# Kernel optimization log

Hardware: AMD Instinct MI355X
Metric: run time of the kernel (lower is better)

The kernel has to match this reference:

```python
import jax, jax.numpy as jnp
import numpy as np

NUM_HEADS = 32
HEAD_DIM = 512
EPS = 1e-12  # torch F.normalize eps


def setup_inputs() -> dict:
    key = jax.random.key(0)
    k1, k2, k3, k4, k5 = jax.random.split(key, 5)
    B, C, H, W = 32, 256, 64, 64
    return {
        "X": jax.random.normal(k1, (B, C, H, W), dtype=jnp.float32),
        "qkv_w": jax.random.normal(k2, (3 * HEAD_DIM, C), dtype=jnp.float32) * 0.02,
        "qkv_b": jax.random.normal(k3, (3 * HEAD_DIM,), dtype=jnp.float32) * 0.02,
        "proj_w": jax.random.normal(k4, (C, HEAD_DIM), dtype=jnp.float32) * 0.02,
        "proj_b": jax.random.normal(k5, (C,), dtype=jnp.float32) * 0.02,
    }


def _l2norm_axis1(x):
    # torch F.normalize(x, dim=1): x / max(||x||_2, eps)
    n = jnp.sqrt(jnp.sum(x * x, axis=1, keepdims=True))
    return x / jnp.maximum(n, EPS)


def reference(X, qkv_w, qkv_b, proj_w, proj_b):
    B, C, H, W = X.shape
    # 1x1 conv == channel matmul: [B,3*hd,H,W]
    qkv = jnp.einsum('bchw,oc->bohw', X, qkv_w) + qkv_b[None, :, None, None]
    # reshape to (B, 3, num_heads, head_dim, L) where L = H*W // num_heads
    qkv = qkv.reshape(B, 3, NUM_HEADS, HEAD_DIM, -1)
    q, k, v = qkv[:, 0], qkv[:, 1], qkv[:, 2]  # [B, nh, hd, L]
    # normalize across the num_heads axis (dim=1), as in the original code
    q = _l2norm_axis1(q)
    k = _l2norm_axis1(k)
    # attn = q^T @ k : [B, nh, L, L]
    attn = jnp.einsum('bhdl,bhdm->bhlm', q, k)
    attn = jax.nn.softmax(attn, axis=-1)
    # output = v @ attn^T : [B, nh, hd, L]
    out = jnp.einsum('bhdm,bhlm->bhdl', v, attn)
    out = out.reshape(B, HEAD_DIM, H, W)
    # proj 1x1 conv back to C channels
    out = jnp.einsum('bdhw,cd->bchw', out, proj_w) + proj_b[None, :, None, None]
    return out
```

## Files before the change

### kernel.cpp

```cpp
#include <hip/hip_runtime.h>
#include <stdint.h>


typedef float     f32x4   __attribute__((ext_vector_type(4)));
typedef short     bf16x8  __attribute__((ext_vector_type(8)));
typedef float     floatx4 __attribute__((ext_vector_type(4)));
typedef uint16_t  ushortx8 __attribute__((ext_vector_type(8)));
typedef uint16_t  ushortx4 __attribute__((ext_vector_type(4)));

#define DEVI static __device__ __forceinline__

DEVI float bf2f(uint16_t u) { union { uint32_t i; float f; } x; x.i = ((uint32_t)u) << 16; return x.f; }
DEVI uint16_t f2bf(float f) {
  union { float f; uint32_t i; } x; x.f = f;
  uint32_t r = x.i + 0x7fff + ((x.i >> 16) & 1);
  return (uint16_t)(r >> 16);
}

DEVI void gload16(const void* g, void* l) {
  __builtin_amdgcn_global_load_lds((const __attribute__((address_space(1))) void*)g,
                                   (__attribute__((address_space(3))) void*)l, 16, 0, 0);
}

DEVI float redmax16(float v) {
  v = fmaxf(v, __shfl_xor(v, 1)); v = fmaxf(v, __shfl_xor(v, 2));
  v = fmaxf(v, __shfl_xor(v, 4)); v = fmaxf(v, __shfl_xor(v, 8));
  return v;
}
DEVI float redsum16(float v) {
  v += __shfl_xor(v, 1); v += __shfl_xor(v, 2);
  v += __shfl_xor(v, 4); v += __shfl_xor(v, 8);
  return v;
}

__global__ __launch_bounds__(256) void k_transpose_x(const float* __restrict__ X,
                                                     uint16_t* __restrict__ Xt) {
  __shared__ float tile[64][65];
  int t = threadIdx.x;
  int st = blockIdx.x, ct = blockIdx.y, b = blockIdx.z;
  int row = t >> 2, cq = t & 3;
  const float* src = X + ((size_t)(b * 256 + ct * 64 + row)) * 4096 + st * 64 + cq * 16;
#pragma unroll
  for (int k = 0; k < 4; ++k) {
    floatx4 v = *(const floatx4*)(src + k * 4);
    tile[row][cq * 16 + k * 4 + 0] = v[0];
    tile[row][cq * 16 + k * 4 + 1] = v[1];
    tile[row][cq * 16 + k * 4 + 2] = v[2];
    tile[row][cq * 16 + k * 4 + 3] = v[3];
  }
  __syncthreads();
  int srow = t >> 2, oq = t & 3;
  ushortx8 o0, o1;
#pragma unroll
  for (int k = 0; k < 8; ++k) o0[k] = f2bf(tile[oq * 16 + k][srow]);
#pragma unroll
  for (int k = 0; k < 8; ++k) o1[k] = f2bf(tile[oq * 16 + 8 + k][srow]);
  uint16_t* dst = Xt + ((size_t)(b * 4096 + st * 64 + srow)) * 256 + ct * 64 + oq * 16;
  *(ushortx8*)dst = o0;
  *(ushortx8*)(dst + 8) = o1;
}

__global__ __launch_bounds__(256) void k_cvt_bf16(const float* __restrict__ src,
                                                  uint16_t* __restrict__ dst, int n) {
  int i = (blockIdx.x * 256 + threadIdx.x) * 4;
  if (i >= n) return;
  floatx4 v = *(const floatx4*)(src + i);
  ushortx4 o;
  o[0] = f2bf(v[0]); o[1] = f2bf(v[1]); o[2] = f2bf(v[2]); o[3] = f2bf(v[3]);
  *(ushortx4*)(dst + i) = o;
}

__global__ __launch_bounds__(256) void k_qkv_gemm(const uint16_t* __restrict__ W,
                                                  const uint16_t* __restrict__ Xt,
                                                  const float* __restrict__ bias_g,
                                                  uint16_t* __restrict__ qkv) {
  __shared__ __align__(16) uint16_t As[128 * 64];
  __shared__ __align__(16) uint16_t Bs[128 * 64];
  int t = threadIdx.x, lane = t & 63, wave = t >> 6;
  int st = blockIdx.x, ot = blockIdx.y, b = blockIdx.z;
  int wr = wave >> 1, wc = wave & 1;
  f32x4 acc[4][4] = {};
  int srow = lane >> 3;
  int sc_us = ((((lane & 7) * 16) ^ ((srow & 7) << 4)) >> 1);
  const uint16_t* Ag = W + (size_t)(ot * 128 + wave * 8 + srow) * 256;
  const uint16_t* Bg = Xt + ((size_t)(b * 4096 + st * 128 + wave * 8 + srow)) * 256;

  for (int kc = 0; kc < 4; ++kc) {
    __syncthreads();
#pragma unroll
    for (int c = 0; c < 4; ++c) {
      gload16(Ag + (size_t)(c * 32) * 256 + kc * 64 + sc_us, &As[(c * 32 + wave * 8) * 64]);
      gload16(Bg + (size_t)(c * 32) * 256 + kc * 64 + sc_us, &Bs[(c * 32 + wave * 8) * 64]);
    }
    __syncthreads();
#pragma unroll
    for (int kk = 0; kk < 2; ++kk) {
      bf16x8 a[4], bw[4];
#pragma unroll
      for (int i = 0; i < 4; ++i) {
        int r = wr * 64 + i * 16 + (lane & 15);
        a[i] = *(const bf16x8*)&As[r * 64 + ((kk * 32 + (lane >> 4) * 8) ^ ((r & 7) << 3))];
      }
#pragma unroll
      for (int j = 0; j < 4; ++j) {
        int r = wc * 64 + j * 16 + (lane & 15);
        bw[j] = *(const bf16x8*)&Bs[r * 64 + ((kk * 32 + (lane >> 4) * 8) ^ ((r & 7) << 3))];
      }
#pragma unroll
      for (int i = 0; i < 4; ++i)
#pragma unroll
        for (int j = 0; j < 4; ++j)
          acc[i][j] = __builtin_amdgcn_mfma_f32_16x16x32_bf16(a[i], bw[j], acc[i][j], 0, 0, 0);
    }
  }
  int o0 = ot * 128 + wr * 64, s0 = st * 128 + wc * 64;
  float bv[4][4];
#pragma unroll
  for (int i = 0; i < 4; ++i)
#pragma unroll
    for (int r = 0; r < 4; ++r) bv[i][r] = bias_g[o0 + i * 16 + (lane >> 4) * 4 + r];
#pragma unroll
  for (int i = 0; i < 4; ++i)
#pragma unroll
    for (int j = 0; j < 4; ++j)
#pragma unroll
      for (int r = 0; r < 4; ++r) {
        int o = o0 + i * 16 + (lane >> 4) * 4 + r;
        int s = s0 + j * 16 + (lane & 15);
        qkv[((size_t)b * 1536 + o) * 4096 + s] = f2bf(acc[i][j][r] + bv[i][r]);
      }
}

__global__ __launch_bounds__(256) void k_scales(const uint16_t* __restrict__ qkv,
                                                float* __restrict__ scaleB) {
  int t = threadIdx.x;
  int sc = blockIdx.x, g = blockIdx.y, b = blockIdx.z;
  const uint16_t* base = qkv + ((size_t)(b * 1536 + g * 512)) * 4096;
  float* sb = scaleB + ((size_t)(b * 2 + g)) * 16 * 4096;
  int c16 = t >> 4, so = t & 15;
  int s = sc * 128 + so * 8;
  float ss[8] = {};
  for (int h = 0; h < 32; ++h) {
    ushortx8 v = *(const ushortx8*)(base + ((size_t)(h * 16 + c16)) * 4096 + s);
#pragma unroll
    for (int j = 0; j < 8; ++j) { float f = bf2f(v[j]); ss[j] += f * f; }
  }
  floatx4 o0, o1;
#pragma unroll
  for (int j = 0; j < 4; ++j) o0[j] = 1.0f / fmaxf(sqrtf(ss[j]), 1e-12f);
#pragma unroll
  for (int j = 0; j < 4; ++j) o1[j] = 1.0f / fmaxf(sqrtf(ss[4 + j]), 1e-12f);
  *(floatx4*)(sb + c16 * 4096 + s) = o0;
  *(floatx4*)(sb + c16 * 4096 + s + 4) = o1;
}

__global__ __launch_bounds__(256) void k_apply(const uint16_t* __restrict__ qkv,
                                               const float* __restrict__ scaleB,
                                               uint16_t* __restrict__ Qp,
                                               uint16_t* __restrict__ Kp) {
  int t = threadIdx.x;
  int shc = blockIdx.x, h = blockIdx.y, z = blockIdx.z;
  int b = z >> 1, g = z & 1;
  const uint16_t* base = qkv + ((size_t)(b * 1536 + g * 512 + h * 16)) * 4096;
  const float* sb = scaleB + ((size_t)(b * 2 + g)) * 16 * 4096;
  uint16_t* dst = (g ? Kp : Qp) + (size_t)b * 32 * 65536 + (size_t)h * 65536;
#pragma unroll
  for (int k = 0; k < 4; ++k) {
    int id = k * 256 + t;
    int l = id & 127, od = id >> 7;
    ushortx8 o;
#pragma unroll
    for (int jj = 0; jj < 8; ++jj) {
      int dp = od * 8 + jj;
      int c16 = dp & 15;
      int s = (shc * 4 + (dp >> 4)) * 128 + l;
      float v = bf2f(base[(size_t)c16 * 4096 + s]);
      o[jj] = f2bf(v * sb[c16 * 4096 + s]);
    }
    *(ushortx8*)(dst + (size_t)l * 512 + shc * 64 + od * 8) = o;
  }
}

__global__ __launch_bounds__(256) void k_attn(const uint16_t* __restrict__ Qp,
                                              const uint16_t* __restrict__ Kp,
                                              const uint16_t* qkv,
                                              uint16_t* OtBase) {
  __shared__ __align__(16) uint16_t smemA[16384];
  __shared__ __align__(16) uint16_t Pb[16384];
  __shared__ float rsum[128];
  int t = threadIdx.x, lane = t & 63, w = t >> 6;
  int h = blockIdx.x, b = blockIdx.y;
  const size_t bh = (size_t)(b * 32 + h);
  const uint16_t* Qg = Qp + bh * 65536;
  const uint16_t* Kg = Kp + bh * 65536;
  uint16_t* QT = smemA;
  uint16_t* KT = smemA + 8192;
  int srow = lane >> 3;
  int sc_us = ((((lane & 7) * 16) ^ ((srow & 7) << 4)) >> 1);

  f32x4 accs[2][8] = {};
  for (int kc = 0; kc < 8; ++kc) {
    __syncthreads();
#pragma unroll
    for (int c = 0; c < 4; ++c) {
      int r = c * 32 + w * 8 + srow;
      gload16(Qg + (size_t)r * 512 + kc * 64 + sc_us, &QT[(c * 32 + w * 8) * 64]);
      gload16(Kg + (size_t)r * 512 + kc * 64 + sc_us, &KT[(c * 32 + w * 8) * 64]);
    }
    __syncthreads();
#pragma unroll
    for (int kk = 0; kk < 2; ++kk) {
      bf16x8 aq[2];
#pragma unroll
      for (int lf = 0; lf < 2; ++lf) {
        int r = w * 32 + lf * 16 + (lane & 15);
        aq[lf] = *(const bf16x8*)&QT[r * 64 + ((kk * 32 + (lane >> 4) * 8) ^ ((r & 7) << 3))];
      }
#pragma unroll
      for (int mf = 0; mf < 8; ++mf) {
        int r = mf * 16 + (lane & 15);
        bf16x8 bk = *(const bf16x8*)&KT[r * 64 + ((kk * 32 + (lane >> 4) * 8) ^ ((r & 7) << 3))];
        accs[0][mf] = __builtin_amdgcn_mfma_f32_16x16x32_bf16(aq[0], bk, accs[0][mf], 0, 0, 0);
        accs[1][mf] = __builtin_amdgcn_mfma_f32_16x16x32_bf16(aq[1], bk, accs[1][mf], 0, 0, 0);
      }
    }
  }

#pragma unroll
  for (int lf = 0; lf < 2; ++lf) {
#pragma unroll
    for (int r = 0; r < 4; ++r) {
      float mx = accs[lf][0][r];
#pragma unroll
      for (int mf = 1; mf < 8; ++mf) mx = fmaxf(mx, accs[lf][mf][r]);
      mx = redmax16(mx);
      float sum = 0.f;
#pragma unroll
      for (int mf = 0; mf < 8; ++mf) {
        float e = __expf(accs[lf][mf][r] - mx);
        accs[lf][mf][r] = e;
        sum += e;
      }
      sum = redsum16(sum);
      int l = w * 32 + lf * 16 + (lane >> 4) * 4 + r;
      if ((lane & 15) == 0) rsum[l] = 1.0f / sum;
#pragma unroll
      for (int mf = 0; mf < 8; ++mf) {
        int m = mf * 16 + (lane & 15);
        Pb[l * 128 + (m ^ ((l & 7) << 3))] = f2bf(accs[lf][mf][r]);
      }
    }
  }
  __syncthreads();

  uint16_t* Vt = smemA;
  const uint16_t* vg = qkv + ((size_t)(b * 1536 + 1024 + h * 16)) * 4096;
  int vrow = lane >> 2;
  int vcol_us = ((((lane & 3) * 16) ^ ((vrow & 3) << 4)) >> 1);
  uint16_t* OtB = OtBase + (size_t)b * 6291456;

#pragma unroll
  for (int lc = 0; lc < 2; ++lc) {
    f32x4 acco[8][4] = {};
    for (int mc = 0; mc < 4; ++mc) {
      __syncthreads();
#pragma unroll
      for (int c = 0; c < 8; ++c) {
        int d = c * 64 + w * 16 + vrow;
        gload16(vg + (size_t)(d >> 5) * 4096 + (d & 31) * 128 + mc * 32 + vcol_us,
                &Vt[(c * 64 + w * 16) * 32]);
      }
      __syncthreads();
      bf16x8 av[8], bp[4];
#pragma unroll
      for (int df = 0; df < 8; ++df) {
        int r = w * 128 + df * 16 + (lane & 15);
        av[df] = *(const bf16x8*)&Vt[r * 32 + (((lane >> 4) * 8) ^ ((r & 3) << 3))];
      }
#pragma unroll
      for (int lf = 0; lf < 4; ++lf) {
        int l = lc * 64 + lf * 16 + (lane & 15);
        bp[lf] = *(const bf16x8*)&Pb[l * 128 + ((mc * 32 + (lane >> 4) * 8) ^ ((l & 7) << 3))];
      }
#pragma unroll
      for (int df = 0; df < 8; ++df)
#pragma unroll
        for (int lf = 0; lf < 4; ++lf)
          acco[df][lf] = __builtin_amdgcn_mfma_f32_16x16x32_bf16(av[df], bp[lf], acco[df][lf], 0, 0, 0);
    }
    float scl[4];
#pragma unroll
    for (int lf = 0; lf < 4; ++lf) scl[lf] = rsum[lc * 64 + lf * 16 + (lane & 15)];

#pragma unroll
    for (int half = 0; half < 2; ++half) {
      __syncthreads();
#pragma unroll
      for (int df = 0; df < 8; ++df)
#pragma unroll
        for (int lf2 = 0; lf2 < 2; ++lf2) {
          int lf = half * 2 + lf2;
          int lloc = lf2 * 16 + (lane & 15);
#pragma unroll
          for (int r = 0; r < 4; ++r) {
            int d = w * 128 + df * 16 + (lane >> 4) * 4 + r;
            Vt[(lloc * 32 + (d & 31)) * 16 + (d >> 5)] = f2bf(acco[df][lf][r] * scl[lf]);
          }
        }
      __syncthreads();
#pragma unroll
      for (int i = 0; i < 4; ++i) {
        int chunk = i * 256 + t;
        int lloc = chunk >> 5, dlo = chunk & 31;
        int l = lc * 64 + half * 32 + lloc;
        ushortx8 v0 = *(ushortx8*)&Vt[chunk * 16];
        ushortx8 v1 = *(ushortx8*)&Vt[chunk * 16 + 8];
        uint16_t* gp = OtB + ((size_t)(dlo * 128 + l)) * 512 + h * 16;
        *(ushortx8*)gp = v0;
        *(ushortx8*)(gp + 8) = v1;
      }
    }
  }
}

__global__ __launch_bounds__(256) void k_proj_gemm(const uint16_t* __restrict__ Wp,
                                                   const uint16_t* __restrict__ Ot,
                                                   const float* __restrict__ bias_g,
                                                   float* __restrict__ outp) {
  __shared__ __align__(16) uint16_t As[128 * 64];
  __shared__ __align__(16) uint16_t Bs[128 * 64];
  int t = threadIdx.x, lane = t & 63, wave = t >> 6;
  int st = blockIdx.x, ct = blockIdx.y, b = blockIdx.z;
  int wr = wave >> 1, wc = wave & 1;
  f32x4 acc[4][4] = {};
  int srow = lane >> 3;
  int sc_us = ((((lane & 7) * 16) ^ ((srow & 7) << 4)) >> 1);
  const uint16_t* Ag = Wp + (size_t)(ct * 128 + wave * 8 + srow) * 512;
  const uint16_t* Bg = Ot + (size_t)b * 6291456 + ((size_t)(st * 128 + wave * 8 + srow)) * 512;

  for (int kc = 0; kc < 8; ++kc) {
    __syncthreads();
#pragma unroll
    for (int c = 0; c < 4; ++c) {
      gload16(Ag + (size_t)(c * 32) * 512 + kc * 64 + sc_us, &As[(c * 32 + wave * 8) * 64]);
      gload16(Bg + (size_t)(c * 32) * 512 + kc * 64 + sc_us, &Bs[(c * 32 + wave * 8) * 64]);
    }
    __syncthreads();
#pragma unroll
    for (int kk = 0; kk < 2; ++kk) {
      bf16x8 a[4], bw[4];
#pragma unroll
      for (int i = 0; i < 4; ++i) {
        int r = wr * 64 + i * 16 + (lane & 15);
        a[i] = *(const bf16x8*)&As[r * 64 + ((kk * 32 + (lane >> 4) * 8) ^ ((r & 7) << 3))];
      }
#pragma unroll
      for (int j = 0; j < 4; ++j) {
        int r = wc * 64 + j * 16 + (lane & 15);
        bw[j] = *(const bf16x8*)&Bs[r * 64 + ((kk * 32 + (lane >> 4) * 8) ^ ((r & 7) << 3))];
      }
#pragma unroll
      for (int i = 0; i < 4; ++i)
#pragma unroll
        for (int j = 0; j < 4; ++j)
          acc[i][j] = __builtin_amdgcn_mfma_f32_16x16x32_bf16(a[i], bw[j], acc[i][j], 0, 0, 0);
    }
  }
  int c0 = ct * 128 + wr * 64, s0 = st * 128 + wc * 64;
  float bv[4][4];
#pragma unroll
  for (int i = 0; i < 4; ++i)
#pragma unroll
    for (int r = 0; r < 4; ++r) bv[i][r] = bias_g[c0 + i * 16 + (lane >> 4) * 4 + r];
#pragma unroll
  for (int i = 0; i < 4; ++i)
#pragma unroll
    for (int j = 0; j < 4; ++j)
#pragma unroll
      for (int r = 0; r < 4; ++r) {
        int c = c0 + i * 16 + (lane >> 4) * 4 + r;
        int s = s0 + j * 16 + (lane & 15);
        outp[((size_t)b * 256 + c) * 4096 + s] = acc[i][j][r] + bv[i][r];
      }
}

extern "C" void kernel_launch(void* const* d_in, const int* in_sizes, int n_in,
                              void* d_out, int out_size, void* d_ws, size_t ws_size,
                              hipStream_t stream) {
  const float* X      = (const float*)d_in[0];
  const float* qkv_w  = (const float*)d_in[1];
  const float* qkv_b  = (const float*)d_in[2];
  const float* proj_w = (const float*)d_in[3];
  const float* proj_b = (const float*)d_in[4];
  float* outp = (float*)d_out;

  const size_t SZ_XT  = 2097152;
  const size_t SZ_QKV = 12582912;
  const size_t SZ_QP  = 4194304;
  const size_t SZ_W   = 786432 + 262144;

  int NB = 0;
  const int cand[6] = {32, 16, 8, 4, 2, 1};
  for (int ci = 0; ci < 6; ++ci) {
    size_t need = SZ_W + (size_t)cand[ci] * (SZ_XT + SZ_QKV + 2 * SZ_QP);
    if (need <= ws_size) { NB = cand[ci]; break; }
  }
  if (NB == 0) return;

  char* ws = (char*)d_ws;
  uint16_t* Wqb  = (uint16_t*)(ws);
  uint16_t* Wpb  = (uint16_t*)(ws + 786432);
  char*     gbuf = ws + SZ_W;
  uint16_t* Xt   = (uint16_t*)(gbuf);
  uint16_t* qkvb = (uint16_t*)(gbuf + (size_t)NB * SZ_XT);
  uint16_t* Qp   = (uint16_t*)(gbuf + (size_t)NB * (SZ_XT + SZ_QKV));
  uint16_t* Kp   = (uint16_t*)(gbuf + (size_t)NB * (SZ_XT + SZ_QKV + SZ_QP));
  float*    scaleB = (float*)Xt;

  k_cvt_bf16<<<dim3(384), 256, 0, stream>>>(qkv_w, Wqb, 1536 * 256);
  k_cvt_bf16<<<dim3(128), 256, 0, stream>>>(proj_w, Wpb, 256 * 512);

  for (int b0 = 0; b0 < 32; b0 += NB) {
    const float* Xg   = X + (size_t)b0 * 256 * 4096;
    float*       outg = outp + (size_t)b0 * 256 * 4096;
    k_transpose_x<<<dim3(64, 4, NB), 256, 0, stream>>>(Xg, Xt);
    k_qkv_gemm<<<dim3(32, 12, NB), 256, 0, stream>>>(Wqb, Xt, qkv_b, qkvb);
    k_scales<<<dim3(32, 2, NB), 256, 0, stream>>>(qkvb, scaleB);
    k_apply<<<dim3(8, 32, 2 * NB), 256, 0, stream>>>(qkvb, scaleB, Qp, Kp);
    k_attn<<<dim3(32, NB), 256, 0, stream>>>(Qp, Kp, qkvb, qkvb );
    k_proj_gemm<<<dim3(32, 2, NB), 256, 0, stream>>>(Wpb, qkvb , proj_b, outg);
  }
}
```

Before: 671.0 us.

## Fuse Q/K normalization into attention and write output in channel-major layout

Removes the separate k_apply pass and its Qp/Kp buffers. The attention kernel now reads bf16 Q/K straight from the qkv buffer, scales them by the precomputed inverse norms and writes them swizzled into LDS. The attention block grows to 512 threads, each wave owning 16 query rows and 64 head dims. The output is written directly in the original channel-major layout without an LDS transpose, and the projection GEMM gathers it with strided scalar loads. This saves a global round trip of Q/K but replaces vectorized async loads with 2-byte scalar gathers in both attention and projection.

Result: faster. 585.2 us (-12.8%).

```diff
diff --git a/kernel.cpp b/kernel.cpp
--- a/kernel.cpp
+++ b/kernel.cpp
@@ -136,7 +136,7 @@
   int t = threadIdx.x;
   int sc = blockIdx.x, g = blockIdx.y, b = blockIdx.z;
   const uint16_t* base = qkv + ((size_t)(b * 1536 + g * 512)) * 4096;
-  float* sb = scaleB + ((size_t)(b * 2 + g)) * 16 * 4096;
+  float* sb = scaleB + (size_t)b * 524288 + (size_t)g * 65536;
   int c16 = t >> 4, so = t & 15;
   int s = sc * 128 + so * 8;
   float ss[8] = {};
@@ -154,177 +154,137 @@
   *(floatx4*)(sb + c16 * 4096 + s + 4) = o1;
 }
 
-__global__ __launch_bounds__(256) void k_apply(const uint16_t* __restrict__ qkv,
-                                               const float* __restrict__ scaleB,
-                                               uint16_t* __restrict__ Qp,
-                                               uint16_t* __restrict__ Kp) {
-  int t = threadIdx.x;
-  int shc = blockIdx.x, h = blockIdx.y, z = blockIdx.z;
-  int b = z >> 1, g = z & 1;
-  const uint16_t* base = qkv + ((size_t)(b * 1536 + g * 512 + h * 16)) * 4096;
-  const float* sb = scaleB + ((size_t)(b * 2 + g)) * 16 * 4096;
-  uint16_t* dst = (g ? Kp : Qp) + (size_t)b * 32 * 65536 + (size_t)h * 65536;
-#pragma unroll
-  for (int k = 0; k < 4; ++k) {
-    int id = k * 256 + t;
-    int l = id & 127, od = id >> 7;
-    ushortx8 o;
-#pragma unroll
-    for (int jj = 0; jj < 8; ++jj) {
-      int dp = od * 8 + jj;
-      int c16 = dp & 15;
-      int s = (shc * 4 + (dp >> 4)) * 128 + l;
-      float v = bf2f(base[(size_t)c16 * 4096 + s]);
-      o[jj] = f2bf(v * sb[c16 * 4096 + s]);
-    }
-    *(ushortx8*)(dst + (size_t)l * 512 + shc * 64 + od * 8) = o;
-  }
-}
-
-__global__ __launch_bounds__(256) void k_attn(const uint16_t* __restrict__ Qp,
-                                              const uint16_t* __restrict__ Kp,
-                                              const uint16_t* qkv,
-                                              uint16_t* OtBase) {
+__global__ __launch_bounds__(512, 4) void k_attn(const uint16_t* __restrict__ qkv,
+                                                 const float* __restrict__ scaleB,
+                                                 uint16_t* OtAll) {
   __shared__ __align__(16) uint16_t smemA[16384];
   __shared__ __align__(16) uint16_t Pb[16384];
   __shared__ float rsum[128];
   int t = threadIdx.x, lane = t & 63, w = t >> 6;
   int h = blockIdx.x, b = blockIdx.y;
-  const size_t bh = (size_t)(b * 32 + h);
-  const uint16_t* Qg = Qp + bh * 65536;
-  const uint16_t* Kg = Kp + bh * 65536;
+  const uint16_t* qg = qkv + ((size_t)(b * 1536) + h * 16) * 4096;
+  const uint16_t* kg = qkv + ((size_t)(b * 1536) + 512 + h * 16) * 4096;
+  const float* sq = scaleB + (size_t)b * 524288;
+  const float* sk = sq + 65536;
   uint16_t* QT = smemA;
   uint16_t* KT = smemA + 8192;
-  int srow = lane >> 3;
-  int sc_us = ((((lane & 7) * 16) ^ ((srow & 7) << 4)) >> 1);
-
-  f32x4 accs[2][8] = {};
+
+  int sl = t & 127;
+  int dd8a = t >> 7;
+
+  f32x4 accs[8] = {};
   for (int kc = 0; kc < 8; ++kc) {
     __syncthreads();
 #pragma unroll
-    for (int c = 0; c < 4; ++c) {
-      int r = c * 32 + w * 8 + srow;
-      gload16(Qg + (size_t)r * 512 + kc * 64 + sc_us, &QT[(c * 32 + w * 8) * 64]);
-      gload16(Kg + (size_t)r * 512 + kc * 64 + sc_us, &KT[(c * 32 + w * 8) * 64]);
+    for (int kq = 0; kq < 2; ++kq) {
+      int dd8 = dd8a + kq * 4;
+      int c16 = kc * 2 + (dd8 >> 2);
+      int s0 = (dd8 & 3) * 8;
+      const uint16_t* qrow = qg + (size_t)c16 * 4096 + sl;
+      const uint16_t* krow = kg + (size_t)c16 * 4096 + sl;
+      const float* sqr = sq + c16 * 4096 + sl;
+      const float* skr = sk + c16 * 4096 + sl;
+      ushortx8 oq, ok;
+#pragma unroll
+      for (int j = 0; j < 8; ++j) {
+        int soff = (s0 + j) * 128;
+        oq[j] = f2bf(bf2f(qrow[soff]) * sqr[soff]);
+        ok[j] = f2bf(bf2f(krow[soff]) * skr[soff]);
+      }
+      int lidx = sl * 64 + ((dd8 * 8) ^ ((sl & 7) << 3));
+      *(ushortx8*)&QT[lidx] = oq;
+      *(ushortx8*)&KT[lidx] = ok;
     }
     __syncthreads();
 #pragma unroll
     for (int kk = 0; kk < 2; ++kk) {
-      bf16x8 aq[2];
-#pragma unroll
-      for (int lf = 0; lf < 2; ++lf) {
-        int r = w * 32 + lf * 16 + (lane & 15);
-        aq[lf] = *(const bf16x8*)&QT[r * 64 + ((kk * 32 + (lane >> 4) * 8) ^ ((r & 7) << 3))];
-      }
+      int ra = w * 16 + (lane & 15);
+      bf16x8 aq = *(const bf16x8*)&QT[ra * 64 + ((kk * 32 + (lane >> 4) * 8) ^ ((ra & 7) << 3))];
 #pragma unroll
       for (int mf = 0; mf < 8; ++mf) {
-        int r = mf * 16 + (lane & 15);
-        bf16x8 bk = *(const bf16x8*)&KT[r * 64 + ((kk * 32 + (lane >> 4) * 8) ^ ((r & 7) << 3))];
-        accs[0][mf] = __builtin_amdgcn_mfma_f32_16x16x32_bf16(aq[0], bk, accs[0][mf], 0, 0, 0);
-        accs[1][mf] = __builtin_amdgcn_mfma_f32_16x16x32_bf16(aq[1], bk, accs[1][mf], 0, 0, 0);
-      }
-    }
-  }
-
-#pragma unroll
-  for (int lf = 0; lf < 2; ++lf) {
-#pragma unroll
-    for (int r = 0; r < 4; ++r) {
-      float mx = accs[lf][0][r];
-#pragma unroll
-      for (int mf = 1; mf < 8; ++mf) mx = fmaxf(mx, accs[lf][mf][r]);
-      mx = redmax16(mx);
-      float sum = 0.f;
-#pragma unroll
-      for (int mf = 0; mf < 8; ++mf) {
-        float e = __expf(accs[lf][mf][r] - mx);
-        accs[lf][mf][r] = e;
-        sum += e;
-      }
-      sum = redsum16(sum);
-      int l = w * 32 + lf * 16 + (lane >> 4) * 4 + r;
-      if ((lane & 15) == 0) rsum[l] = 1.0f / sum;
-#pragma unroll
-      for (int mf = 0; mf < 8; ++mf) {
-        int m = mf * 16 + (lane & 15);
-        Pb[l * 128 + (m ^ ((l & 7) << 3))] = f2bf(accs[lf][mf][r]);
-      }
+        int rm = mf * 16 + (lane & 15);
+        bf16x8 bk = *(const bf16x8*)&KT[rm * 64 + ((kk * 32 + (lane >> 4) * 8) ^ ((rm & 7) << 3))];
+        accs[mf] = __builtin_amdgcn_mfma_f32_16x16x32_bf16(aq, bk, accs[mf], 0, 0, 0);
+      }
+    }
+  }
+
+#pragma unroll
+  for (int r = 0; r < 4; ++r) {
+    float mx = accs[0][r];
+#pragma unroll
+    for (int mf = 1; mf < 8; ++mf) mx = fmaxf(mx, accs[mf][r]);
+    mx = redmax16(mx);
+    float sum = 0.f;
+#pragma unroll
+    for (int mf = 0; mf < 8; ++mf) {
+      float e = __expf(accs[mf][r] - mx);
+      accs[mf][r] = e;
+      sum += e;
+    }
+    sum = redsum16(sum);
+    int l = w * 16 + (lane >> 4) * 4 + r;
+    if ((lane & 15) == 0) rsum[l] = 1.0f / sum;
+#pragma unroll
+    for (int mf = 0; mf < 8; ++mf) {
+      int m = mf * 16 + (lane & 15);
+      Pb[l * 128 + (m ^ ((l & 7) << 3))] = f2bf(accs[mf][r]);
     }
   }
   __syncthreads();
 
-  uint16_t* Vt = smemA;
-  const uint16_t* vg = qkv + ((size_t)(b * 1536 + 1024 + h * 16)) * 4096;
+  const uint16_t* vg = qkv + ((size_t)(b * 1536) + 1024 + h * 16) * 4096;
+  uint16_t* OtT = OtAll + (size_t)b * 6291456;
   int vrow = lane >> 2;
   int vcol_us = ((((lane & 3) * 16) ^ ((vrow & 3) << 4)) >> 1);
-  uint16_t* OtB = OtBase + (size_t)b * 6291456;
 
 #pragma unroll
   for (int lc = 0; lc < 2; ++lc) {
-    f32x4 acco[8][4] = {};
+    f32x4 acco[4][4] = {};
     for (int mc = 0; mc < 4; ++mc) {
       __syncthreads();
 #pragma unroll
-      for (int c = 0; c < 8; ++c) {
-        int d = c * 64 + w * 16 + vrow;
+      for (int c = 0; c < 4; ++c) {
+        int d = w * 64 + c * 16 + vrow;
         gload16(vg + (size_t)(d >> 5) * 4096 + (d & 31) * 128 + mc * 32 + vcol_us,
-                &Vt[(c * 64 + w * 16) * 32]);
+                &smemA[(w * 64 + c * 16) * 32]);
       }
       __syncthreads();
-      bf16x8 av[8], bp[4];
-#pragma unroll
-      for (int df = 0; df < 8; ++df) {
-        int r = w * 128 + df * 16 + (lane & 15);
-        av[df] = *(const bf16x8*)&Vt[r * 32 + (((lane >> 4) * 8) ^ ((r & 3) << 3))];
-      }
+      bf16x8 bp[4];
 #pragma unroll
       for (int lf = 0; lf < 4; ++lf) {
         int l = lc * 64 + lf * 16 + (lane & 15);
         bp[lf] = *(const bf16x8*)&Pb[l * 128 + ((mc * 32 + (lane >> 4) * 8) ^ ((l & 7) << 3))];
       }
 #pragma unroll
-      for (int df = 0; df < 8; ++df)
+      for (int df = 0; df < 4; ++df) {
+        int rv = w * 64 + df * 16 + (lane & 15);
+        bf16x8 av = *(const bf16x8*)&smemA[rv * 32 + (((lane >> 4) * 8) ^ ((rv & 3) << 3))];
 #pragma unroll
         for (int lf = 0; lf < 4; ++lf)
-          acco[df][lf] = __builtin_amdgcn_mfma_f32_16x16x32_bf16(av[df], bp[lf], acco[df][lf], 0, 0, 0);
+          acco[df][lf] = __builtin_amdgcn_mfma_f32_16x16x32_bf16(av, bp[lf], acco[df][lf], 0, 0, 0);
+      }
     }
     float scl[4];
 #pragma unroll
     for (int lf = 0; lf < 4; ++lf) scl[lf] = rsum[lc * 64 + lf * 16 + (lane & 15)];
-
-#pragma unroll
-    for (int half = 0; half < 2; ++half) {
-      __syncthreads();
-#pragma unroll
-      for (int df = 0; df < 8; ++df)
-#pragma unroll
-        for (int lf2 = 0; lf2 < 2; ++lf2) {
-          int lf = half * 2 + lf2;
-          int lloc = lf2 * 16 + (lane & 15);
-#pragma unroll
-          for (int r = 0; r < 4; ++r) {
-            int d = w * 128 + df * 16 + (lane >> 4) * 4 + r;
-            Vt[(lloc * 32 + (d & 31)) * 16 + (d >> 5)] = f2bf(acco[df][lf][r] * scl[lf]);
-          }
+#pragma unroll
+    for (int df = 0; df < 4; ++df)
+#pragma unroll
+      for (int r = 0; r < 4; ++r) {
+        int d = w * 64 + df * 16 + (lane >> 4) * 4 + r;
+        uint16_t* orow = OtT + ((size_t)(h * 16 + (d >> 5))) * 4096 + (d & 31) * 128;
+#pragma unroll
+        for (int lf = 0; lf < 4; ++lf) {
+          int l = lc * 64 + lf * 16 + (lane & 15);
+          orow[l] = f2bf(acco[df][lf][r] * scl[lf]);
         }
-      __syncthreads();
-#pragma unroll
-      for (int i = 0; i < 4; ++i) {
-        int chunk = i * 256 + t;
-        int lloc = chunk >> 5, dlo = chunk & 31;
-        int l = lc * 64 + half * 32 + lloc;
-        ushortx8 v0 = *(ushortx8*)&Vt[chunk * 16];
-        ushortx8 v1 = *(ushortx8*)&Vt[chunk * 16 + 8];
-        uint16_t* gp = OtB + ((size_t)(dlo * 128 + l)) * 512 + h * 16;
-        *(ushortx8*)gp = v0;
-        *(ushortx8*)(gp + 8) = v1;
-      }
-    }
+      }
   }
 }
 
 __global__ __launch_bounds__(256) void k_proj_gemm(const uint16_t* __restrict__ Wp,
-                                                   const uint16_t* __restrict__ Ot,
+                                                   const uint16_t* __restrict__ OtAll,
                                                    const float* __restrict__ bias_g,
                                                    float* __restrict__ outp) {
   __shared__ __align__(16) uint16_t As[128 * 64];
@@ -336,14 +296,22 @@
   int srow = lane >> 3;
   int sc_us = ((((lane & 7) * 16) ^ ((srow & 7) << 4)) >> 1);
   const uint16_t* Ag = Wp + (size_t)(ct * 128 + wave * 8 + srow) * 512;
-  const uint16_t* Bg = Ot + (size_t)b * 6291456 + ((size_t)(st * 128 + wave * 8 + srow)) * 512;
+  const uint16_t* Ob = OtAll + (size_t)b * 6291456;
 
   for (int kc = 0; kc < 8; ++kc) {
     __syncthreads();
 #pragma unroll
-    for (int c = 0; c < 4; ++c) {
+    for (int c = 0; c < 4; ++c)
       gload16(Ag + (size_t)(c * 32) * 512 + kc * 64 + sc_us, &As[(c * 32 + wave * 8) * 64]);
-      gload16(Bg + (size_t)(c * 32) * 512 + kc * 64 + sc_us, &Bs[(c * 32 + wave * 8) * 64]);
+#pragma unroll
+    for (int k = 0; k < 4; ++k) {
+      int cid = k * 256 + t;
+      int row = cid & 127, dd8 = cid >> 7;
+      const uint16_t* src = Ob + (size_t)(kc * 64 + dd8 * 8) * 4096 + st * 128 + row;
+      ushortx8 o;
+#pragma unroll
+      for (int j = 0; j < 8; ++j) o[j] = src[(size_t)j * 4096];
+      *(ushortx8*)&Bs[row * 64 + ((dd8 * 8) ^ ((row & 7) << 3))] = o;
     }
     __syncthreads();
 #pragma unroll
@@ -396,13 +364,12 @@
 
   const size_t SZ_XT  = 2097152;
   const size_t SZ_QKV = 12582912;
-  const size_t SZ_QP  = 4194304;
   const size_t SZ_W   = 786432 + 262144;
 
   int NB = 0;
   const int cand[6] = {32, 16, 8, 4, 2, 1};
   for (int ci = 0; ci < 6; ++ci) {
-    size_t need = SZ_W + (size_t)cand[ci] * (SZ_XT + SZ_QKV + 2 * SZ_QP);
+    size_t need = SZ_W + (size_t)cand[ci] * (SZ_XT + SZ_QKV);
     if (need <= ws_size) { NB = cand[ci]; break; }
   }
   if (NB == 0) return;
@@ -413,8 +380,6 @@
   char*     gbuf = ws + SZ_W;
   uint16_t* Xt   = (uint16_t*)(gbuf);
   uint16_t* qkvb = (uint16_t*)(gbuf + (size_t)NB * SZ_XT);
-  uint16_t* Qp   = (uint16_t*)(gbuf + (size_t)NB * (SZ_XT + SZ_QKV));
-  uint16_t* Kp   = (uint16_t*)(gbuf + (size_t)NB * (SZ_XT + SZ_QKV + SZ_QP));
   float*    scaleB = (float*)Xt;
 
   k_cvt_bf16<<<dim3(384), 256, 0, stream>>>(qkv_w, Wqb, 1536 * 256);
@@ -426,8 +391,7 @@
     k_transpose_x<<<dim3(64, 4, NB), 256, 0, stream>>>(Xg, Xt);
     k_qkv_gemm<<<dim3(32, 12, NB), 256, 0, stream>>>(Wqb, Xt, qkv_b, qkvb);
     k_scales<<<dim3(32, 2, NB), 256, 0, stream>>>(qkvb, scaleB);
-    k_apply<<<dim3(8, 32, 2 * NB), 256, 0, stream>>>(qkvb, scaleB, Qp, Kp);
-    k_attn<<<dim3(32, NB), 256, 0, stream>>>(Qp, Kp, qkvb, qkvb );
+    k_attn<<<dim3(32, NB), 512, 0, stream>>>(qkvb, scaleB, qkvb );
     k_proj_gemm<<<dim3(32, 2, NB), 256, 0, stream>>>(Wpb, qkvb , proj_b, outg);
   }
 }
```
